# Optimization experiments

Hardware: AMD Instinct MI355X
Metric: run time of the kernel (lower is better)

## Reference

```python
import jax, jax.numpy as jnp
import numpy as np

N = 100000      # nodes
E = 1600000     # edges (avg degree 16)
IN = 512        # in_channels
H = 256         # hidden_channels
L = 8           # num_layers
ALPHA = 0.1
THETA = 0.5


def setup_inputs() -> dict:
    key = jax.random.key(0)
    k0, k1, k2, k3 = jax.random.split(key, 4)
    x = jax.random.normal(k0, (N, IN), jnp.float32)
    edge_index = jax.random.randint(k1, (2, E), 0, N, dtype=jnp.int64)
    W_embed = jax.random.normal(k2, (IN, H), jnp.float32) / np.sqrt(IN)
    b_embed = jnp.zeros((H,), jnp.float32)
    W_convs = jax.random.normal(k3, (L, H, H), jnp.float32) / np.sqrt(H)
    return {"x": x, "edge_index": edge_index, "W_embed": W_embed,
            "b_embed": b_embed, "W_convs": W_convs}


def _gcn_norm(edge_index, n):
    # gcn_norm: A_hat = A + I, D^{-1/2} A_hat D^{-1/2}
    loop = jnp.arange(n, dtype=edge_index.dtype)
    row = jnp.concatenate([edge_index[0], loop])  # source
    col = jnp.concatenate([edge_index[1], loop])  # target
    ones = jnp.ones(row.shape[0], jnp.float32)
    deg = jax.ops.segment_sum(ones, col, num_segments=n)
    dinv = jnp.where(deg > 0, jax.lax.rsqrt(deg), 0.0)
    norm = dinv[row] * dinv[col]  # [E+N]
    return row, col, norm


def _propagate(x, row, col, norm, n):
    # SpMM: out[i] = sum_{(j->i)} norm_e * x[j]
    msgs = x[row] * norm[:, None]  # [E+N, H]
    return jax.ops.segment_sum(msgs, col, num_segments=n)


def _gcn2_conv(x, x0, row, col, norm, W, layer):
    beta = np.log(THETA / layer + 1.0)
    h = _propagate(x, row, col, norm, x.shape[0])
    h = (1.0 - ALPHA) * h + ALPHA * x0          # initial residual (shared_weights)
    return (1.0 - beta) * h + beta * (h @ W)    # identity mapping


def reference(x, edge_index, W_embed, b_embed, W_convs):
    n = x.shape[0]
    row, col, norm = _gcn_norm(edge_index, n)
    h = jax.nn.relu(x @ W_embed + b_embed)
    h0 = h
    for l in range(L - 1):
        h = _gcn2_conv(h, h0, row, col, norm, W_convs[l], layer=l + 1)
        h = jax.nn.relu(h)  # dropout is identity in eval mode
    h = _gcn2_conv(h, h0, row, col, norm, W_convs[L - 1], layer=L)
    return h
```

## Files before the change

kernel.cpp:

```cpp
#include <hip/hip_runtime.h>
#include <cmath>

#define NNODES 100000
#define NEDGES 1600000
#define INC 512
#define HC 256
#define NLAYERS 8

typedef _Float16 half8 __attribute__((ext_vector_type(8)));
typedef _Float16 half4v __attribute__((ext_vector_type(4)));
typedef float floatx4 __attribute__((ext_vector_type(4)));

struct __attribute__((aligned(8))) EdgeP { int s; float w; };

__global__ void k_detect(const unsigned int* __restrict__ eb, int* __restrict__ mode) {
  int lane = threadIdx.x;
  unsigned v = eb[2 * lane + 1];
  unsigned long long nz = __ballot(v != 0u);
  if (lane == 0) *mode = (nz == 0ull) ? 1 : 0;
}

__device__ __forceinline__ int edge_at(const void* eb, int m, int i) {
  return m ? (int)((const long long*)eb)[i] : ((const int*)eb)[i];
}


__global__ __launch_bounds__(256) void k_zero2(int* __restrict__ a, int* __restrict__ b, int n) {
  int i = blockIdx.x * 256 + threadIdx.x;
  if (i < n) { a[i] = 0; b[i] = 0; }
}

__global__ __launch_bounds__(256) void k_count(const void* __restrict__ eb, const int* __restrict__ mode,
                                               int* __restrict__ counts) {
  int e = blockIdx.x * 256 + threadIdx.x;
  if (e >= NEDGES) return;
  int m = *mode;
  atomicAdd(&counts[edge_at(eb, m, NEDGES + e)], 1);
}

__global__ __launch_bounds__(256) void k_dinv(const int* __restrict__ counts, float* __restrict__ dinv) {
  int i = blockIdx.x * 256 + threadIdx.x;
  if (i < NNODES) dinv[i] = 1.0f / sqrtf((float)counts[i] + 1.0f);
}

__global__ __launch_bounds__(256) void k_scan1(const int* __restrict__ counts, int* __restrict__ rowptr,
                                               int* __restrict__ partials) {
  __shared__ int sm[256];
  int i = blockIdx.x * 256 + threadIdx.x;
  int v = (i < NNODES) ? counts[i] : 0;
  sm[threadIdx.x] = v;
  __syncthreads();
  for (int off = 1; off < 256; off <<= 1) {
    int u = (threadIdx.x >= off) ? sm[threadIdx.x - off] : 0;
    __syncthreads();
    sm[threadIdx.x] += u;
    __syncthreads();
  }
  if (i < NNODES) rowptr[i] = sm[threadIdx.x] - v;
  if (threadIdx.x == 255) partials[blockIdx.x] = sm[255];
}

__global__ __launch_bounds__(512) void k_scan2(int* __restrict__ partials, int* __restrict__ rowptr, int nb) {
  __shared__ int sm[512];
  int t = threadIdx.x;
  int v = (t < nb) ? partials[t] : 0;
  sm[t] = v;
  __syncthreads();
  for (int off = 1; off < 512; off <<= 1) {
    int u = (t >= off) ? sm[t - off] : 0;
    __syncthreads();
    sm[t] += u;
    __syncthreads();
  }
  if (t < nb) partials[t] = sm[t] - v;
  if (t == 0) rowptr[NNODES] = NEDGES;
}

__global__ __launch_bounds__(256) void k_scan3(int* __restrict__ rowptr, const int* __restrict__ partials) {
  int i = blockIdx.x * 256 + threadIdx.x;
  if (i < NNODES) rowptr[i] += partials[blockIdx.x];
}

__global__ __launch_bounds__(256) void k_fill(const void* __restrict__ eb, const int* __restrict__ mode,
                                              const int* __restrict__ rowptr,
                                              int* __restrict__ cursor, const float* __restrict__ dinv,
                                              EdgeP* __restrict__ ep) {
  int e = blockIdx.x * 256 + threadIdx.x;
  if (e >= NEDGES) return;
  int m = *mode;
  int r = edge_at(eb, m, e), c = edge_at(eb, m, NEDGES + e);
  int p = rowptr[c] + atomicAdd(&cursor[c], 1);
  EdgeP pr; pr.s = r; pr.w = dinv[r] * dinv[c];
  ep[p] = pr;
}

__global__ __launch_bounds__(256) void k_tr_wemb(const float* __restrict__ W, _Float16* __restrict__ WT) {
  int idx = blockIdx.x * 256 + threadIdx.x;
  int k = idx & 511, c = idx >> 9;
  WT[idx] = (_Float16)W[k * 256 + c];
}
__global__ __launch_bounds__(256) void k_tr_wc(const float* __restrict__ W, _Float16* __restrict__ WT) {
  int idx = blockIdx.x * 256 + threadIdx.x;
  int k = idx & 255, n = (idx >> 8) & 255, l = idx >> 16;
  WT[idx] = (_Float16)W[(l * 256 + k) * 256 + n];
}


template <int K, bool AF16, bool BIAS, bool ID, bool RELU, bool F16OUT>
__global__ __launch_bounds__(256) void k_dense(const void* A, const _Float16* __restrict__ WT,
                                               const float* __restrict__ bias,
                                               const void* mfid,
                                               float ob, float beta,
                                               _Float16* __restrict__ outh, _Float16* __restrict__ outh2,
                                               float* outf) {
  int t = threadIdx.x;
  int wave = t >> 6, lane = t & 63;
  int r = lane & 15, g = lane >> 4;
  int row0 = blockIdx.x * 64;
  int c0 = wave * 64;
  int ar[4];
#pragma unroll
  for (int rt = 0; rt < 4; ++rt) {
    int rr = row0 + rt * 16 + r;
    ar[rt] = (rr < NNODES) ? rr : (NNODES - 1);
  }

  auto loadA = [&](half8 (&a)[4], int ks) {
#pragma unroll
    for (int rt = 0; rt < 4; ++rt) {
      if constexpr (AF16) {
        a[rt] = *(const half8*)((const _Float16*)A + (size_t)ar[rt] * K + ks + g * 8);
      } else {
        const float* ap = (const float*)A + (size_t)ar[rt] * K + ks + g * 8;
        float4 p0 = *(const float4*)ap;
        float4 p1 = *(const float4*)(ap + 4);
        a[rt] = half8{ (_Float16)p0.x, (_Float16)p0.y, (_Float16)p0.z, (_Float16)p0.w,
                       (_Float16)p1.x, (_Float16)p1.y, (_Float16)p1.z, (_Float16)p1.w };
      }
    }
  };
  auto loadB = [&](half8 (&b)[4], int ks) {
#pragma unroll
    for (int ct = 0; ct < 4; ++ct)
      b[ct] = *(const half8*)(WT + (size_t)(c0 + ct * 16 + r) * K + ks + g * 8);
  };

  floatx4 acc[4][4] = {};
  half8 aP[4], bP[4], aQ[4], bQ[4];
  loadA(aP, 0); loadB(bP, 0);
#pragma unroll
  for (int ks = 0; ks < K; ks += 64) {
    loadA(aQ, ks + 32); loadB(bQ, ks + 32);
#pragma unroll
    for (int rt = 0; rt < 4; ++rt)
#pragma unroll
      for (int ct = 0; ct < 4; ++ct)
        acc[rt][ct] = __builtin_amdgcn_mfma_f32_16x16x32_f16(aP[rt], bP[ct], acc[rt][ct], 0, 0, 0);
    if (ks + 64 < K) { loadA(aP, ks + 64); loadB(bP, ks + 64); }
#pragma unroll
    for (int rt = 0; rt < 4; ++rt)
#pragma unroll
      for (int ct = 0; ct < 4; ++ct)
        acc[rt][ct] = __builtin_amdgcn_mfma_f32_16x16x32_f16(aQ[rt], bQ[ct], acc[rt][ct], 0, 0, 0);
  }

  auto idval = [&](size_t off) -> float {
    if constexpr (AF16) return (float)((const _Float16*)mfid)[off];
    else return ((const float*)mfid)[off];
  };

  if constexpr (!F16OUT) {
    __syncthreads();
#pragma unroll
    for (int rt = 0; rt < 4; ++rt) {
#pragma unroll
      for (int q = 0; q < 4; ++q) {
        int row = row0 + rt * 16 + g * 4 + q;
        if (row >= NNODES) continue;
#pragma unroll
        for (int ct = 0; ct < 4; ++ct) {
          int col = c0 + ct * 16 + r;
          size_t off = (size_t)row * HC + col;
          float v = acc[rt][ct][q];
          if constexpr (ID) v = ob * idval(off) + beta * v;
          if constexpr (BIAS) v += bias[col];
          if constexpr (RELU) v = fmaxf(v, 0.0f);
          outf[off] = v;
        }
      }
    }
  } else {
    __shared__ _Float16 Cl[64][264];
#pragma unroll
    for (int rt = 0; rt < 4; ++rt) {
#pragma unroll
      for (int q = 0; q < 4; ++q) {
        int lrow = rt * 16 + g * 4 + q;
        int row = row0 + lrow;
        int crow = (row < NNODES) ? row : (NNODES - 1);
#pragma unroll
        for (int ct = 0; ct < 4; ++ct) {
          int col = c0 + ct * 16 + r;
          float v = acc[rt][ct][q];
          if constexpr (ID) v = ob * idval((size_t)crow * HC + col) + beta * v;
          if constexpr (BIAS) v += bias[col];
          if constexpr (RELU) v = fmaxf(v, 0.0f);
          Cl[lrow][col] = (_Float16)v;
        }
      }
    }
    __syncthreads();
    int lrow = t >> 2, cc = (t & 3) * 64;
    int grow = row0 + lrow;
    if (grow < NNODES) {
      size_t base = (size_t)grow * HC + cc;
#pragma unroll
      for (int i = 0; i < 8; ++i) {
        half8 v = *(const half8*)&Cl[lrow][cc + i * 8];
        *(half8*)(outh + base + i * 8) = v;
        if (outh2) *(half8*)(outh2 + base + i * 8) = v;
      }
    }
  }
}


template <bool LAST>
__global__ __launch_bounds__(256) void k_layer(const _Float16* __restrict__ h,
                                               const _Float16* __restrict__ h0,
                                               const int* __restrict__ rowptr,
                                               const EdgeP* __restrict__ ep,
                                               const float* __restrict__ dinv,
                                               const _Float16* __restrict__ WT,
                                               float ob, float beta,
                                               _Float16* __restrict__ hn, float* __restrict__ outf) {
  __shared__ _Float16 M[32][264];
  int t = threadIdx.x;
  int wave = t >> 6, lane = t & 63;
  int row0 = blockIdx.x * 32;
  int c = lane * 4;

  for (int i = 0; i < 8; ++i) {
    int lrow = wave * 8 + i;
    int node = row0 + lrow;
    if (node < NNODES) {
      size_t base = (size_t)node * HC + c;
      float di = dinv[node];
      float wsw = di * di;
      half4v hv = *(const half4v*)(h + base);
      float a0 = wsw * (float)hv[0], a1 = wsw * (float)hv[1];
      float a2 = wsw * (float)hv[2], a3 = wsw * (float)hv[3];
      int e = rowptr[node], en = rowptr[node + 1];
      for (; e + 7 < en; e += 8) {
        EdgeP p0 = ep[e],     p1 = ep[e + 1], p2 = ep[e + 2], p3 = ep[e + 3];
        EdgeP p4 = ep[e + 4], p5 = ep[e + 5], p6 = ep[e + 6], p7 = ep[e + 7];
        half4v x0 = *(const half4v*)(h + (size_t)p0.s * HC + c);
        half4v x1 = *(const half4v*)(h + (size_t)p1.s * HC + c);
        half4v x2 = *(const half4v*)(h + (size_t)p2.s * HC + c);
        half4v x3 = *(const half4v*)(h + (size_t)p3.s * HC + c);
        half4v x4 = *(const half4v*)(h + (size_t)p4.s * HC + c);
        half4v x5 = *(const half4v*)(h + (size_t)p5.s * HC + c);
        half4v x6 = *(const half4v*)(h + (size_t)p6.s * HC + c);
        half4v x7 = *(const half4v*)(h + (size_t)p7.s * HC + c);
        a0 += p0.w * (float)x0[0] + p1.w * (float)x1[0] + p2.w * (float)x2[0] + p3.w * (float)x3[0]
            + p4.w * (float)x4[0] + p5.w * (float)x5[0] + p6.w * (float)x6[0] + p7.w * (float)x7[0];
        a1 += p0.w * (float)x0[1] + p1.w * (float)x1[1] + p2.w * (float)x2[1] + p3.w * (float)x3[1]
            + p4.w * (float)x4[1] + p5.w * (float)x5[1] + p6.w * (float)x6[1] + p7.w * (float)x7[1];
        a2 += p0.w * (float)x0[2] + p1.w * (float)x1[2] + p2.w * (float)x2[2] + p3.w * (float)x3[2]
            + p4.w * (float)x4[2] + p5.w * (float)x5[2] + p6.w * (float)x6[2] + p7.w * (float)x7[2];
        a3 += p0.w * (float)x0[3] + p1.w * (float)x1[3] + p2.w * (float)x2[3] + p3.w * (float)x3[3]
            + p4.w * (float)x4[3] + p5.w * (float)x5[3] + p6.w * (float)x6[3] + p7.w * (float)x7[3];
      }
      for (; e + 3 < en; e += 4) {
        EdgeP p0 = ep[e], p1 = ep[e + 1], p2 = ep[e + 2], p3 = ep[e + 3];
        half4v x0 = *(const half4v*)(h + (size_t)p0.s * HC + c);
        half4v x1 = *(const half4v*)(h + (size_t)p1.s * HC + c);
        half4v x2 = *(const half4v*)(h + (size_t)p2.s * HC + c);
        half4v x3 = *(const half4v*)(h + (size_t)p3.s * HC + c);
        a0 += p0.w * (float)x0[0] + p1.w * (float)x1[0] + p2.w * (float)x2[0] + p3.w * (float)x3[0];
        a1 += p0.w * (float)x0[1] + p1.w * (float)x1[1] + p2.w * (float)x2[1] + p3.w * (float)x3[1];
        a2 += p0.w * (float)x0[2] + p1.w * (float)x1[2] + p2.w * (float)x2[2] + p3.w * (float)x3[2];
        a3 += p0.w * (float)x0[3] + p1.w * (float)x1[3] + p2.w * (float)x2[3] + p3.w * (float)x3[3];
      }
      for (; e < en; ++e) {
        EdgeP p0 = ep[e];
        half4v x0 = *(const half4v*)(h + (size_t)p0.s * HC + c);
        a0 += p0.w * (float)x0[0];
        a1 += p0.w * (float)x0[1];
        a2 += p0.w * (float)x0[2];
        a3 += p0.w * (float)x0[3];
      }
      half4v h0v = *(const half4v*)(h0 + base);
      half4v mo = { (_Float16)(0.9f * a0 + 0.1f * (float)h0v[0]),
                    (_Float16)(0.9f * a1 + 0.1f * (float)h0v[1]),
                    (_Float16)(0.9f * a2 + 0.1f * (float)h0v[2]),
                    (_Float16)(0.9f * a3 + 0.1f * (float)h0v[3]) };
      *(half4v*)&M[lrow][c] = mo;
    } else {
      *(half4v*)&M[lrow][c] = half4v{ (_Float16)0, (_Float16)0, (_Float16)0, (_Float16)0 };
    }
  }
  __syncthreads();

  int r = lane & 15, g = lane >> 4;
  int c0 = wave * 64;
  floatx4 acc[2][4] = {};
#pragma unroll
  for (int ks = 0; ks < HC; ks += 32) {
    half8 a[2], b[4];
    a[0] = *(const half8*)&M[r][ks + g * 8];
    a[1] = *(const half8*)&M[16 + r][ks + g * 8];
#pragma unroll
    for (int ct = 0; ct < 4; ++ct)
      b[ct] = *(const half8*)(WT + (size_t)(c0 + ct * 16 + r) * HC + ks + g * 8);
#pragma unroll
    for (int rt = 0; rt < 2; ++rt)
#pragma unroll
      for (int ct = 0; ct < 4; ++ct)
        acc[rt][ct] = __builtin_amdgcn_mfma_f32_16x16x32_f16(a[rt], b[ct], acc[rt][ct], 0, 0, 0);
  }
  __syncthreads();

#pragma unroll
  for (int rt = 0; rt < 2; ++rt) {
#pragma unroll
    for (int q = 0; q < 4; ++q) {
      int lrow = rt * 16 + g * 4 + q;
#pragma unroll
      for (int ct = 0; ct < 4; ++ct) {
        int col = c0 + ct * 16 + r;
        float v = ob * (float)M[lrow][col] + beta * acc[rt][ct][q];
        if constexpr (!LAST) {
          v = fmaxf(v, 0.0f);
          M[lrow][col] = (_Float16)v;
        } else {
          int row = row0 + lrow;
          if (row < NNODES) outf[(size_t)row * HC + col] = v;
        }
      }
    }
  }
  if constexpr (!LAST) {
    __syncthreads();
    int lrow = t >> 3, cc = (t & 7) * 32;
    int grow = row0 + lrow;
    if (grow < NNODES) {
      size_t base = (size_t)grow * HC + cc;
#pragma unroll
      for (int i = 0; i < 4; ++i)
        *(half8*)(hn + base + i * 8) = *(const half8*)&M[lrow][cc + i * 8];
    }
  }
}


extern "C" void kernel_launch(void* const* d_in, const int* in_sizes, int n_in,
                              void* d_out, int out_size, void* d_ws, size_t ws_size,
                              hipStream_t stream) {
  const float* x = (const float*)d_in[0];
  const void* ei = d_in[1];
  const float* wemb = (const float*)d_in[2];
  const float* bemb = (const float*)d_in[3];
  const float* wc = (const float*)d_in[4];
  (void)in_sizes; (void)n_in; (void)out_size; (void)ws_size;

  char* ws = (char*)d_ws;
  size_t o = 0;
  auto alloc = [&](size_t bytes) -> char* {
    char* p = ws + o;
    o = (o + bytes + 511) & ~(size_t)511;
    return p;
  };
  _Float16* hh      = (_Float16*)alloc((size_t)NNODES * HC * 2);
  _Float16* h0h     = (_Float16*)alloc((size_t)NNODES * HC * 2);
  EdgeP*    ep      = (EdgeP*)alloc((size_t)NEDGES * 8);
  _Float16* wembT   = (_Float16*)alloc((size_t)INC * HC * 2);
  _Float16* wcT     = (_Float16*)alloc((size_t)NLAYERS * HC * HC * 2);
  int*      counts  = (int*)alloc((size_t)NNODES * 4);
  int*      cursor  = (int*)alloc((size_t)NNODES * 4);
  int*      rowptr  = (int*)alloc((size_t)(NNODES + 1) * 4);
  float*    dinv    = (float*)alloc((size_t)NNODES * 4);
  int*      partials= (int*)alloc(2048);
  int*      mode    = (int*)alloc(256);
  _Float16* hd      = (_Float16*)d_out;

  const int NB = (NNODES + 255) / 256;
  const int GEMM_GRID = (NNODES + 63) / 64;
  const int LAYER_GRID = (NNODES + 31) / 32;

  k_detect<<<1, 64, 0, stream>>>((const unsigned int*)ei, mode);
  k_zero2<<<NB, 256, 0, stream>>>(counts, cursor, NNODES);
  k_tr_wemb<<<(INC * HC) / 256, 256, 0, stream>>>(wemb, wembT);
  k_tr_wc<<<(NLAYERS * HC * HC) / 256, 256, 0, stream>>>(wc, wcT);
  k_count<<<(NEDGES + 255) / 256, 256, 0, stream>>>(ei, mode, counts);
  k_dinv<<<NB, 256, 0, stream>>>(counts, dinv);
  k_scan1<<<NB, 256, 0, stream>>>(counts, rowptr, partials);
  k_scan2<<<1, 512, 0, stream>>>(partials, rowptr, NB);
  k_scan3<<<NB, 256, 0, stream>>>(rowptr, partials);
  k_fill<<<(NEDGES + 255) / 256, 256, 0, stream>>>(ei, mode, rowptr, cursor, dinv, ep);

  k_dense<INC, false, true, false, true, true><<<GEMM_GRID, 256, 0, stream>>>(
      x, wembT, bemb, (const void*)nullptr, 0.0f, 1.0f, hd, h0h, (float*)nullptr);

  _Float16* cur = hd;
  _Float16* nxt = hh;
  for (int l = 0; l < NLAYERS; ++l) {
    float beta = (float)log(0.5 / (double)(l + 1) + 1.0);
    float ob = 1.0f - beta;
    const _Float16* W = wcT + (size_t)l * HC * HC;
    if (l < NLAYERS - 1) {
      k_layer<false><<<LAYER_GRID, 256, 0, stream>>>(cur, h0h, rowptr, ep, dinv, W,
                                                     ob, beta, nxt, (float*)nullptr);
      _Float16* tmp = cur; cur = nxt; nxt = tmp;
    } else {
      k_layer<true><<<LAYER_GRID, 256, 0, stream>>>(cur, h0h, rowptr, ep, dinv, W,
                                                    ob, beta, (_Float16*)nullptr, (float*)d_out);
    }
  }
}
```

Before: 1.932 ms.

## Stage embed GEMM input through LDS with async loads; nontemporal edge loads

Replaces the generic templated dense kernel with a dedicated embedding GEMM that double-buffers fp32 X tiles into swizzled shared memory via global_load_lds, then converts to fp16 for MFMA. The epilogue is split into two passes to fit the smaller LDS buffer. Separately, the per-layer SpMM now reads edge records and h0 with nontemporal loads so these streamed data do not evict the gathered feature rows from cache. Risks include extra barriers per k-step and reduced register-level prefetch of B.

```diff
diff --git a/kernel.cpp b/kernel.cpp
--- a/kernel.cpp
+++ b/kernel.cpp
@@ -11,7 +11,19 @@
 typedef _Float16 half4v __attribute__((ext_vector_type(4)));
 typedef float floatx4 __attribute__((ext_vector_type(4)));
 
+typedef __attribute__((address_space(3))) unsigned int u32_lds;
+typedef __attribute__((address_space(1))) unsigned int u32_glb;
+
 struct __attribute__((aligned(8))) EdgeP { int s; float w; };
+
+__device__ __forceinline__ EdgeP ldnt_edge(const EdgeP* p) {
+  unsigned long long v = __builtin_nontemporal_load((const unsigned long long*)p);
+  EdgeP e; __builtin_memcpy(&e, &v, 8); return e;
+}
+__device__ __forceinline__ half4v ldnt_h4(const _Float16* p) {
+  unsigned long long v = __builtin_nontemporal_load((const unsigned long long*)p);
+  half4v h; __builtin_memcpy(&h, &v, 8); return h;
+}
 
 __global__ void k_detect(const unsigned int* __restrict__ eb, int* __restrict__ mode) {
   int lane = threadIdx.x;
@@ -106,119 +118,92 @@
 }
 
 
-template <int K, bool AF16, bool BIAS, bool ID, bool RELU, bool F16OUT>
-__global__ __launch_bounds__(256) void k_dense(const void* A, const _Float16* __restrict__ WT,
+__global__ __launch_bounds__(256) void k_embed(const float* __restrict__ X,
+                                               const _Float16* __restrict__ WT,
                                                const float* __restrict__ bias,
-                                               const void* mfid,
-                                               float ob, float beta,
-                                               _Float16* __restrict__ outh, _Float16* __restrict__ outh2,
-                                               float* outf) {
+                                               _Float16* __restrict__ outh, _Float16* __restrict__ outh2) {
+  __shared__ char smem[16896];
   int t = threadIdx.x;
   int wave = t >> 6, lane = t & 63;
   int r = lane & 15, g = lane >> 4;
   int row0 = blockIdx.x * 64;
   int c0 = wave * 64;
-  int ar[4];
-#pragma unroll
-  for (int rt = 0; rt < 4; ++rt) {
-    int rr = row0 + rt * 16 + r;
-    ar[rt] = (rr < NNODES) ? rr : (NNODES - 1);
-  }
-
-  auto loadA = [&](half8 (&a)[4], int ks) {
+
+  floatx4 acc[4][4] = {};
+
+  auto stage = [&](int buf, int ks) {
+#pragma unroll
+    for (int rd = 0; rd < 2; ++rd) {
+      int L = rd * 256 + t;
+      int row = L >> 3;
+      int u = (L & 7) ^ (row & 7);
+      int grow = row0 + row; if (grow >= NNODES) grow = NNODES - 1;
+      const float* src = X + (size_t)grow * INC + ks + u * 4;
+      char* dstbase = smem + buf * 8192 + (rd * 256 + wave * 64) * 16;
+      __builtin_amdgcn_global_load_lds((const u32_glb*)src, (u32_lds*)dstbase, 16, 0, 0);
+    }
+  };
+
+  auto compute = [&](int buf, int ks) {
+    const char* bufp = smem + buf * 8192;
+    half8 a[4], b[4];
 #pragma unroll
     for (int rt = 0; rt < 4; ++rt) {
-      if constexpr (AF16) {
-        a[rt] = *(const half8*)((const _Float16*)A + (size_t)ar[rt] * K + ks + g * 8);
-      } else {
-        const float* ap = (const float*)A + (size_t)ar[rt] * K + ks + g * 8;
-        float4 p0 = *(const float4*)ap;
-        float4 p1 = *(const float4*)(ap + 4);
-        a[rt] = half8{ (_Float16)p0.x, (_Float16)p0.y, (_Float16)p0.z, (_Float16)p0.w,
-                       (_Float16)p1.x, (_Float16)p1.y, (_Float16)p1.z, (_Float16)p1.w };
-      }
-    }
+      int row = rt * 16 + r;
+      int sw = row & 7;
+      float4 f0 = *(const float4*)(bufp + row * 128 + ((2 * g) ^ sw) * 16);
+      float4 f1 = *(const float4*)(bufp + row * 128 + ((2 * g + 1) ^ sw) * 16);
+      a[rt] = half8{ (_Float16)f0.x, (_Float16)f0.y, (_Float16)f0.z, (_Float16)f0.w,
+                     (_Float16)f1.x, (_Float16)f1.y, (_Float16)f1.z, (_Float16)f1.w };
+    }
+#pragma unroll
+    for (int ct = 0; ct < 4; ++ct)
+      b[ct] = *(const half8*)(WT + (size_t)(c0 + ct * 16 + r) * INC + ks + g * 8);
+#pragma unroll
+    for (int rt = 0; rt < 4; ++rt)
+#pragma unroll
+      for (int ct = 0; ct < 4; ++ct)
+        acc[rt][ct] = __builtin_amdgcn_mfma_f32_16x16x32_f16(a[rt], b[ct], acc[rt][ct], 0, 0, 0);
   };
-  auto loadB = [&](half8 (&b)[4], int ks) {
-#pragma unroll
-    for (int ct = 0; ct < 4; ++ct)
-      b[ct] = *(const half8*)(WT + (size_t)(c0 + ct * 16 + r) * K + ks + g * 8);
-  };
-
-  floatx4 acc[4][4] = {};
-  half8 aP[4], bP[4], aQ[4], bQ[4];
-  loadA(aP, 0); loadB(bP, 0);
-#pragma unroll
-  for (int ks = 0; ks < K; ks += 64) {
-    loadA(aQ, ks + 32); loadB(bQ, ks + 32);
-#pragma unroll
-    for (int rt = 0; rt < 4; ++rt)
-#pragma unroll
-      for (int ct = 0; ct < 4; ++ct)
-        acc[rt][ct] = __builtin_amdgcn_mfma_f32_16x16x32_f16(aP[rt], bP[ct], acc[rt][ct], 0, 0, 0);
-    if (ks + 64 < K) { loadA(aP, ks + 64); loadB(bP, ks + 64); }
-#pragma unroll
-    for (int rt = 0; rt < 4; ++rt)
-#pragma unroll
-      for (int ct = 0; ct < 4; ++ct)
-        acc[rt][ct] = __builtin_amdgcn_mfma_f32_16x16x32_f16(aQ[rt], bQ[ct], acc[rt][ct], 0, 0, 0);
-  }
-
-  auto idval = [&](size_t off) -> float {
-    if constexpr (AF16) return (float)((const _Float16*)mfid)[off];
-    else return ((const float*)mfid)[off];
-  };
-
-  if constexpr (!F16OUT) {
-    __syncthreads();
-#pragma unroll
-    for (int rt = 0; rt < 4; ++rt) {
+
+  stage(0, 0);
+#pragma unroll 2
+  for (int s = 0; s < 16; ++s) {
+    if (s < 15) stage((s + 1) & 1, (s + 1) * 32);
+    __syncthreads();
+    compute(s & 1, s * 32);
+    __syncthreads();
+  }
+
+  _Float16 (*Cl)[264] = (_Float16(*)[264])smem;
+#pragma unroll
+  for (int p = 0; p < 2; ++p) {
+    __syncthreads();
+#pragma unroll
+    for (int rt2 = 0; rt2 < 2; ++rt2) {
+      int rt = p * 2 + rt2;
 #pragma unroll
       for (int q = 0; q < 4; ++q) {
-        int row = row0 + rt * 16 + g * 4 + q;
-        if (row >= NNODES) continue;
+        int lrow = rt2 * 16 + g * 4 + q;
 #pragma unroll
         for (int ct = 0; ct < 4; ++ct) {
           int col = c0 + ct * 16 + r;
-          size_t off = (size_t)row * HC + col;
-          float v = acc[rt][ct][q];
-          if constexpr (ID) v = ob * idval(off) + beta * v;
-          if constexpr (BIAS) v += bias[col];
-          if constexpr (RELU) v = fmaxf(v, 0.0f);
-          outf[off] = v;
-        }
-      }
-    }
-  } else {
-    __shared__ _Float16 Cl[64][264];
-#pragma unroll
-    for (int rt = 0; rt < 4; ++rt) {
-#pragma unroll
-      for (int q = 0; q < 4; ++q) {
-        int lrow = rt * 16 + g * 4 + q;
-        int row = row0 + lrow;
-        int crow = (row < NNODES) ? row : (NNODES - 1);
-#pragma unroll
-        for (int ct = 0; ct < 4; ++ct) {
-          int col = c0 + ct * 16 + r;
-          float v = acc[rt][ct][q];
-          if constexpr (ID) v = ob * idval((size_t)crow * HC + col) + beta * v;
-          if constexpr (BIAS) v += bias[col];
-          if constexpr (RELU) v = fmaxf(v, 0.0f);
+          float v = acc[rt][ct][q] + bias[col];
+          v = fmaxf(v, 0.0f);
           Cl[lrow][col] = (_Float16)v;
         }
       }
     }
     __syncthreads();
-    int lrow = t >> 2, cc = (t & 3) * 64;
-    int grow = row0 + lrow;
+    int lrow = t >> 3, cc = (t & 7) * 32;
+    int grow = row0 + p * 32 + lrow;
     if (grow < NNODES) {
       size_t base = (size_t)grow * HC + cc;
 #pragma unroll
-      for (int i = 0; i < 8; ++i) {
+      for (int i = 0; i < 4; ++i) {
         half8 v = *(const half8*)&Cl[lrow][cc + i * 8];
         *(half8*)(outh + base + i * 8) = v;
-        if (outh2) *(half8*)(outh2 + base + i * 8) = v;
+        *(half8*)(outh2 + base + i * 8) = v;
       }
     }
   }
@@ -252,8 +237,10 @@
       float a2 = wsw * (float)hv[2], a3 = wsw * (float)hv[3];
       int e = rowptr[node], en = rowptr[node + 1];
       for (; e + 7 < en; e += 8) {
-        EdgeP p0 = ep[e],     p1 = ep[e + 1], p2 = ep[e + 2], p3 = ep[e + 3];
-        EdgeP p4 = ep[e + 4], p5 = ep[e + 5], p6 = ep[e + 6], p7 = ep[e + 7];
+        EdgeP p0 = ldnt_edge(ep + e),     p1 = ldnt_edge(ep + e + 1);
+        EdgeP p2 = ldnt_edge(ep + e + 2), p3 = ldnt_edge(ep + e + 3);
+        EdgeP p4 = ldnt_edge(ep + e + 4), p5 = ldnt_edge(ep + e + 5);
+        EdgeP p6 = ldnt_edge(ep + e + 6), p7 = ldnt_edge(ep + e + 7);
         half4v x0 = *(const half4v*)(h + (size_t)p0.s * HC + c);
         half4v x1 = *(const half4v*)(h + (size_t)p1.s * HC + c);
         half4v x2 = *(const half4v*)(h + (size_t)p2.s * HC + c);
@@ -272,7 +259,8 @@
             + p4.w * (float)x4[3] + p5.w * (float)x5[3] + p6.w * (float)x6[3] + p7.w * (float)x7[3];
       }
       for (; e + 3 < en; e += 4) {
-        EdgeP p0 = ep[e], p1 = ep[e + 1], p2 = ep[e + 2], p3 = ep[e + 3];
+        EdgeP p0 = ldnt_edge(ep + e),     p1 = ldnt_edge(ep + e + 1);
+        EdgeP p2 = ldnt_edge(ep + e + 2), p3 = ldnt_edge(ep + e + 3);
         half4v x0 = *(const half4v*)(h + (size_t)p0.s * HC + c);
         half4v x1 = *(const half4v*)(h + (size_t)p1.s * HC + c);
         half4v x2 = *(const half4v*)(h + (size_t)p2.s * HC + c);
@@ -283,14 +271,14 @@
         a3 += p0.w * (float)x0[3] + p1.w * (float)x1[3] + p2.w * (float)x2[3] + p3.w * (float)x3[3];
       }
       for (; e < en; ++e) {
-        EdgeP p0 = ep[e];
+        EdgeP p0 = ldnt_edge(ep + e);
         half4v x0 = *(const half4v*)(h + (size_t)p0.s * HC + c);
         a0 += p0.w * (float)x0[0];
         a1 += p0.w * (float)x0[1];
         a2 += p0.w * (float)x0[2];
         a3 += p0.w * (float)x0[3];
       }
-      half4v h0v = *(const half4v*)(h0 + base);
+      half4v h0v = ldnt_h4(h0 + base);
       half4v mo = { (_Float16)(0.9f * a0 + 0.1f * (float)h0v[0]),
                     (_Float16)(0.9f * a1 + 0.1f * (float)h0v[1]),
                     (_Float16)(0.9f * a2 + 0.1f * (float)h0v[2]),
@@ -399,8 +387,7 @@
   k_scan3<<<NB, 256, 0, stream>>>(rowptr, partials);
   k_fill<<<(NEDGES + 255) / 256, 256, 0, stream>>>(ei, mode, rowptr, cursor, dinv, ep);
 
-  k_dense<INC, false, true, false, true, true><<<GEMM_GRID, 256, 0, stream>>>(
-      x, wembT, bemb, (const void*)nullptr, 0.0f, 1.0f, hd, h0h, (float*)nullptr);
+  k_embed<<<GEMM_GRID, 256, 0, stream>>>(x, wembT, bemb, hd, h0h);
 
   _Float16* cur = hd;
   _Float16* nxt = hh;
```

After: 1.954 ms. No clear change (+1.1%).
